# Kernel optimization log

Measured on AMD Instinct MI355X. Metric: run time of the kernel, lower is better.

## Reference

```python
import jax, jax.numpy as jnp
import numpy as np

ACT_BITS = 8  # global_act_bit in the original repo
QMAX = float(2 ** ACT_BITS - 1)


def _fake_quant_asym(x):
    """Asymmetric per-tensor fake quantization (weight_quant_fn, activate=True)."""
    mx = jnp.max(x)
    mn = jnp.min(x)
    scale = (mx - mn) / QMAX
    zp = jnp.round(-mn / scale)
    q = jnp.clip(jnp.round(x / scale) + zp, 0.0, QMAX)
    return (q - zp) * scale


def setup_inputs() -> dict:
    key = jax.random.key(0)
    kx, kq, kr, kl, ks = jax.random.split(key, 5)
    B, S, IN, OUT, R = 32, 1024, 1152, 1152, 64
    x = jax.random.normal(kx, (B, S, IN), dtype=jnp.float32)
    quant_w = jax.random.normal(kq, (OUT, IN), dtype=jnp.float32) * 0.02  # quant.weight
    right_w = jax.random.normal(kr, (R, IN), dtype=jnp.float32) * 0.02   # right.weight
    left_w = jax.random.normal(kl, (OUT, R), dtype=jnp.float32) * 0.02   # left.weight
    bias = jnp.zeros((OUT,), dtype=jnp.float32)
    scales = jax.random.uniform(ks, (IN,), dtype=jnp.float32, minval=0.5, maxval=2.0)
    return {"x": x, "quant_w": quant_w, "right_w": right_w,
            "left_w": left_w, "bias": bias, "scales": scales}


def reference(x, quant_w, right_w, left_w, bias, scales):
    # inference path, merge=False: smooth-quant style scale division, then
    # asymmetric per-tensor fake quant, then quant GEMM + low-rank SVD adapter.
    xs = x / scales                                   # [B,S,IN] elementwise
    xq = _fake_quant_asym(xs)                         # global max/min fake quant
    hx = jnp.einsum('bsi,oi->bso', xq, quant_w)       # quantized linear
    lrx = jnp.einsum('bsr,or->bso',
                     jnp.einsum('bsi,ri->bsr', xq, right_w), left_w)  # low-rank
    return hx + lrx + bias
```

## Files before the change

### kernel.cpp

```cpp
#include <hip/hip_runtime.h>
#include <hip/hip_bf16.h>
#include <stdint.h>

#define M_DIM   32768
#define IN_DIM  1152
#define OUT_DIM 1152
#define R_DIM   64
#define QMAXF   255.0f

#define MM_BLOCKS 2048
#define WP_BLOCKS (OUT_DIM * IN_DIM / 256)
#define QBLOCKS   4096

typedef float  f32x4  __attribute__((ext_vector_type(4)));
typedef __bf16 bf16x8 __attribute__((ext_vector_type(8)));

static __device__ __forceinline__ unsigned short f2bf(float f) {
    unsigned int u = __float_as_uint(f);
    unsigned int r = (u + 0x7fffu + ((u >> 16) & 1u)) >> 16;
    return (unsigned short)r;
}

__global__ __launch_bounds__(256) void k_prep(const float* __restrict__ x,
                                              const float* __restrict__ scales,
                                              const float* __restrict__ qw,
                                              const float* __restrict__ rw,
                                              const float* __restrict__ lw,
                                              unsigned short* __restrict__ wc,
                                              float* __restrict__ rs,
                                              float* __restrict__ partials) {
    __shared__ __align__(16) float srs[IN_DIM];
    __shared__ float smn[4], smx[4];

    if (blockIdx.x < MM_BLOCKS) {
        for (int c = threadIdx.x; c < IN_DIM; c += 256)
            srs[c] = 1.0f / scales[c];
        __syncthreads();

        const int n4 = (M_DIM * IN_DIM) / 4;
        int tid = blockIdx.x * 256 + threadIdx.x;
        const int stride = MM_BLOCKS * 256;
        float mn = 3.4e38f, mx = -3.4e38f;
        for (int i4 = tid; i4 < n4; i4 += stride) {
            int i = i4 * 4;
            float4 xv = *(const float4*)(x + i);
            int c = i % IN_DIM;
            float4 sv = *(const float4*)(&srs[c]);
            float a0 = xv.x * sv.x, a1 = xv.y * sv.y;
            float a2 = xv.z * sv.z, a3 = xv.w * sv.w;
            mn = fminf(mn, fminf(fminf(a0, a1), fminf(a2, a3)));
            mx = fmaxf(mx, fmaxf(fmaxf(a0, a1), fmaxf(a2, a3)));
        }
        #pragma unroll
        for (int off = 32; off > 0; off >>= 1) {
            mn = fminf(mn, __shfl_down(mn, off));
            mx = fmaxf(mx, __shfl_down(mx, off));
        }
        int lane = threadIdx.x & 63, wv = threadIdx.x >> 6;
        if (lane == 0) { smn[wv] = mn; smx[wv] = mx; }
        __syncthreads();
        if (threadIdx.x == 0) {
            float bmn = fminf(fminf(smn[0], smn[1]), fminf(smn[2], smn[3]));
            float bmx = fmaxf(fmaxf(smx[0], smx[1]), fmaxf(smx[2], smx[3]));
            partials[blockIdx.x * 2]     = bmn;
            partials[blockIdx.x * 2 + 1] = bmx;
        }
    } else {
        int idx = (blockIdx.x - MM_BLOCKS) * 256 + threadIdx.x;
        if (idx < IN_DIM) rs[idx] = 1.0f / scales[idx];
        int o = idx / IN_DIM;
        int i = idx - o * IN_DIM;
        float acc = qw[idx];
        #pragma unroll 8
        for (int r = 0; r < R_DIM; r++)
            acc += lw[o * R_DIM + r] * rw[r * IN_DIM + i];
        wc[idx] = f2bf(acc);
    }
}

__global__ __launch_bounds__(256) void k_quantf(const float* __restrict__ x,
                                                const float* __restrict__ rs,
                                                const float* __restrict__ partials,
                                                float* __restrict__ qp,
                                                unsigned short* __restrict__ xq) {
    __shared__ float smn[4], smx[4];
    __shared__ float s_lo, s_hi, s_rqs;

    float mn = 3.4e38f, mx = -3.4e38f;
    for (int i = threadIdx.x; i < MM_BLOCKS; i += 256) {
        mn = fminf(mn, partials[i * 2]);
        mx = fmaxf(mx, partials[i * 2 + 1]);
    }
    #pragma unroll
    for (int off = 32; off > 0; off >>= 1) {
        mn = fminf(mn, __shfl_down(mn, off));
        mx = fmaxf(mx, __shfl_down(mx, off));
    }
    int lane = threadIdx.x & 63, wv = threadIdx.x >> 6;
    if (lane == 0) { smn[wv] = mn; smx[wv] = mx; }
    __syncthreads();
    if (threadIdx.x == 0) {
        float bmn = fminf(fminf(smn[0], smn[1]), fminf(smn[2], smn[3]));
        float bmx = fmaxf(fmaxf(smx[0], smx[1]), fmaxf(smx[2], smx[3]));
        float qs = (bmx - bmn) / QMAXF;
        float zp = rintf(-bmn / qs);
        s_lo  = -zp;
        s_hi  = QMAXF - zp;
        s_rqs = 1.0f / qs;
        if (blockIdx.x == 0) qp[0] = qs;
    }
    __syncthreads();
    const float lo = s_lo, hi = s_hi, rqs = s_rqs;

    const int n4 = (M_DIM * IN_DIM) / 4;
    int tid = blockIdx.x * 256 + threadIdx.x;
    const int stride = QBLOCKS * 256;
    for (int i4 = tid; i4 < n4; i4 += stride) {
        int i = i4 * 4;
        float4 xv = *(const float4*)(x + i);
        int c = i % IN_DIM;
        float4 sv = *(const float4*)(rs + c);
        float a[4] = { (xv.x * sv.x) * rqs, (xv.y * sv.y) * rqs,
                       (xv.z * sv.z) * rqs, (xv.w * sv.w) * rqs };
        ushort4 o;
        unsigned short* op = (unsigned short*)&o;
        #pragma unroll
        for (int j = 0; j < 4; j++) {
            float q = rintf(a[j]);
            q = fminf(fmaxf(q, lo), hi);
            op[j] = f2bf(q);
        }
        *(ushort4*)(xq + i) = o;
    }
}

#define BM 128
#define BN 128
#define BK 32

__global__ __launch_bounds__(256) void k_gemm(const unsigned short* __restrict__ A,
                                              const unsigned short* __restrict__ Bw,
                                              const float* __restrict__ bias,
                                              const float* __restrict__ qp,
                                              float* __restrict__ C) {
    __shared__ __align__(16) unsigned short As[BM * BK];
    __shared__ __align__(16) unsigned short Bs[BN * BK];
    const int tid = threadIdx.x;
    const int bm = blockIdx.x, bn = blockIdx.y;
    const int K = IN_DIM, N = OUT_DIM;

    const int r0 = tid >> 2;
    const int c0 = (tid & 3) * 8;
    const unsigned short* ga0 = A  + (size_t)(bm * BM + r0) * K + c0;
    const unsigned short* ga1 = ga0 + (size_t)64 * K;
    const unsigned short* gb0 = Bw + (size_t)(bn * BN + r0) * K + c0;
    const unsigned short* gb1 = gb0 + (size_t)64 * K;
    unsigned short* lA0 = As + tid * 8;
    unsigned short* lA1 = As + tid * 8 + 2048;
    unsigned short* lB0 = Bs + tid * 8;
    unsigned short* lB1 = Bs + tid * 8 + 2048;

    f32x4 acc[4][4];
    #pragma unroll
    for (int mi = 0; mi < 4; mi++)
        #pragma unroll
        for (int ni = 0; ni < 4; ni++)
            acc[mi][ni] = (f32x4)0.0f;

    const int lane = tid & 63, wv = tid >> 6;
    const int wm = (wv & 1) * 64;
    const int wn = (wv >> 1) * 64;
    const int l16 = lane & 15, l4 = lane >> 4;
    const bf16x8* Asv = (const bf16x8*)As;
    const bf16x8* Bsv = (const bf16x8*)Bs;
    const int afo = (wm + l16) * 4 + l4;
    const int bfo = (wn + l16) * 4 + l4;

    for (int k0 = 0; k0 < K; k0 += BK) {
        __builtin_amdgcn_global_load_lds(
            (const __attribute__((address_space(1))) unsigned int*)(ga0 + k0),
            (__attribute__((address_space(3))) unsigned int*)lA0, 16, 0, 0);
        __builtin_amdgcn_global_load_lds(
            (const __attribute__((address_space(1))) unsigned int*)(ga1 + k0),
            (__attribute__((address_space(3))) unsigned int*)lA1, 16, 0, 0);
        __builtin_amdgcn_global_load_lds(
            (const __attribute__((address_space(1))) unsigned int*)(gb0 + k0),
            (__attribute__((address_space(3))) unsigned int*)lB0, 16, 0, 0);
        __builtin_amdgcn_global_load_lds(
            (const __attribute__((address_space(1))) unsigned int*)(gb1 + k0),
            (__attribute__((address_space(3))) unsigned int*)lB1, 16, 0, 0);
        __syncthreads();

        bf16x8 af[4], bf[4];
        #pragma unroll
        for (int mi = 0; mi < 4; mi++) af[mi] = Asv[afo + mi * 64];
        #pragma unroll
        for (int ni = 0; ni < 4; ni++) bf[ni] = Bsv[bfo + ni * 64];
        #pragma unroll
        for (int mi = 0; mi < 4; mi++)
            #pragma unroll
            for (int ni = 0; ni < 4; ni++)
                acc[mi][ni] = __builtin_amdgcn_mfma_f32_16x16x32_bf16(
                    af[mi], bf[ni], acc[mi][ni], 0, 0, 0);
        __syncthreads();
    }

    const float qs = qp[0];
    #pragma unroll
    for (int mi = 0; mi < 4; mi++) {
        int row0 = bm * BM + wm + mi * 16 + l4 * 4;
        #pragma unroll
        for (int ni = 0; ni < 4; ni++) {
            int col = bn * BN + wn + ni * 16 + l16;
            float bv = bias[col];
            #pragma unroll
            for (int r = 0; r < 4; r++)
                C[(size_t)(row0 + r) * N + col] = acc[mi][ni][r] * qs + bv;
        }
    }
}

extern "C" void kernel_launch(void* const* d_in, const int* in_sizes, int n_in,
                              void* d_out, int out_size, void* d_ws, size_t ws_size,
                              hipStream_t stream) {
    const float* x      = (const float*)d_in[0];
    const float* qw     = (const float*)d_in[1];
    const float* rw     = (const float*)d_in[2];
    const float* lw     = (const float*)d_in[3];
    const float* bias   = (const float*)d_in[4];
    const float* scales = (const float*)d_in[5];

    char* ws = (char*)d_ws;
    unsigned short* xq = (unsigned short*)ws;
    unsigned short* wc = (unsigned short*)(ws + 75497472);
    float* partials    = (float*)(ws + 75497472 + 2654208);
    float* qp          = (float*)(ws + 75497472 + 2654208 + 16384);
    float* rs          = (float*)(ws + 75497472 + 2654208 + 16384 + 64);

    k_prep  <<<MM_BLOCKS + WP_BLOCKS, 256, 0, stream>>>(x, scales, qw, rw, lw,
                                                        wc, rs, partials);
    k_quantf<<<QBLOCKS, 256, 0, stream>>>(x, rs, partials, qp, xq);

    dim3 grid(M_DIM / BM, OUT_DIM / BN);
    k_gemm<<<grid, 256, 0, stream>>>(xq, wc, bias, qp, (float*)d_out);
}
```

Baseline: 418.1 us.

## Swizzle LDS tiles, overlap next-tile loads with MFMA, vectorize epilogue stores

The GEMM now XOR-swizzles the LDS column chunk per row pair to reduce bank conflicts on fragment reads. It issues the global-to-LDS loads for the next K tile right after the fragments are pulled into registers, so the loads overlap with that tile's MFMAs, still using a single buffer. The MFMA operands are swapped so each lane holds four consecutive columns, which lets the epilogue write float4 stores and read bias as a vector. The cost is an extra barrier per iteration, and the single LDS buffer leaves only the MFMA work to hide load latency.

```diff
diff --git a/kernel.cpp b/kernel.cpp
--- a/kernel.cpp
+++ b/kernel.cpp
@@ -137,6 +137,7 @@
 #define BM 128
 #define BN 128
 #define BK 32
+#define NT (IN_DIM / BK)
 
 __global__ __launch_bounds__(256) void k_gemm(const unsigned short* __restrict__ A,
                                               const unsigned short* __restrict__ Bw,
@@ -150,7 +151,7 @@
     const int K = IN_DIM, N = OUT_DIM;
 
     const int r0 = tid >> 2;
-    const int c0 = (tid & 3) * 8;
+    const int c0 = (((tid & 3) ^ ((r0 >> 1) & 3))) * 8;
     const unsigned short* ga0 = A  + (size_t)(bm * BM + r0) * K + c0;
     const unsigned short* ga1 = ga0 + (size_t)64 * K;
     const unsigned short* gb0 = Bw + (size_t)(bn * BN + r0) * K + c0;
@@ -173,22 +174,24 @@
     const int l16 = lane & 15, l4 = lane >> 4;
     const bf16x8* Asv = (const bf16x8*)As;
     const bf16x8* Bsv = (const bf16x8*)Bs;
-    const int afo = (wm + l16) * 4 + l4;
-    const int bfo = (wn + l16) * 4 + l4;
-
-    for (int k0 = 0; k0 < K; k0 += BK) {
-        __builtin_amdgcn_global_load_lds(
-            (const __attribute__((address_space(1))) unsigned int*)(ga0 + k0),
-            (__attribute__((address_space(3))) unsigned int*)lA0, 16, 0, 0);
-        __builtin_amdgcn_global_load_lds(
-            (const __attribute__((address_space(1))) unsigned int*)(ga1 + k0),
-            (__attribute__((address_space(3))) unsigned int*)lA1, 16, 0, 0);
-        __builtin_amdgcn_global_load_lds(
-            (const __attribute__((address_space(1))) unsigned int*)(gb0 + k0),
-            (__attribute__((address_space(3))) unsigned int*)lB0, 16, 0, 0);
-        __builtin_amdgcn_global_load_lds(
-            (const __attribute__((address_space(1))) unsigned int*)(gb1 + k0),
-            (__attribute__((address_space(3))) unsigned int*)lB1, 16, 0, 0);
+    const int swz = ((l16 >> 1) & 3);
+    const int afo = (wm + l16) * 4 + (l4 ^ swz);
+    const int bfo = (wn + l16) * 4 + (l4 ^ swz);
+
+    __builtin_amdgcn_global_load_lds(
+        (const __attribute__((address_space(1))) unsigned int*)ga0,
+        (__attribute__((address_space(3))) unsigned int*)lA0, 16, 0, 0);
+    __builtin_amdgcn_global_load_lds(
+        (const __attribute__((address_space(1))) unsigned int*)ga1,
+        (__attribute__((address_space(3))) unsigned int*)lA1, 16, 0, 0);
+    __builtin_amdgcn_global_load_lds(
+        (const __attribute__((address_space(1))) unsigned int*)gb0,
+        (__attribute__((address_space(3))) unsigned int*)lB0, 16, 0, 0);
+    __builtin_amdgcn_global_load_lds(
+        (const __attribute__((address_space(1))) unsigned int*)gb1,
+        (__attribute__((address_space(3))) unsigned int*)lB1, 16, 0, 0);
+
+    for (int t = 0; t < NT; ++t) {
         __syncthreads();
 
         bf16x8 af[4], bf[4];
@@ -196,26 +199,49 @@
         for (int mi = 0; mi < 4; mi++) af[mi] = Asv[afo + mi * 64];
         #pragma unroll
         for (int ni = 0; ni < 4; ni++) bf[ni] = Bsv[bfo + ni * 64];
+
+        __syncthreads();
+
+        if (t + 1 < NT) {
+            const int kc = (t + 1) * BK;
+            __builtin_amdgcn_global_load_lds(
+                (const __attribute__((address_space(1))) unsigned int*)(ga0 + kc),
+                (__attribute__((address_space(3))) unsigned int*)lA0, 16, 0, 0);
+            __builtin_amdgcn_global_load_lds(
+                (const __attribute__((address_space(1))) unsigned int*)(ga1 + kc),
+                (__attribute__((address_space(3))) unsigned int*)lA1, 16, 0, 0);
+            __builtin_amdgcn_global_load_lds(
+                (const __attribute__((address_space(1))) unsigned int*)(gb0 + kc),
+                (__attribute__((address_space(3))) unsigned int*)lB0, 16, 0, 0);
+            __builtin_amdgcn_global_load_lds(
+                (const __attribute__((address_space(1))) unsigned int*)(gb1 + kc),
+                (__attribute__((address_space(3))) unsigned int*)lB1, 16, 0, 0);
+        }
+
         #pragma unroll
         for (int mi = 0; mi < 4; mi++)
             #pragma unroll
             for (int ni = 0; ni < 4; ni++)
                 acc[mi][ni] = __builtin_amdgcn_mfma_f32_16x16x32_bf16(
-                    af[mi], bf[ni], acc[mi][ni], 0, 0, 0);
-        __syncthreads();
+                    bf[ni], af[mi], acc[mi][ni], 0, 0, 0);
     }
 
     const float qs = qp[0];
     #pragma unroll
     for (int mi = 0; mi < 4; mi++) {
-        int row0 = bm * BM + wm + mi * 16 + l4 * 4;
+        const int row = bm * BM + wm + mi * 16 + l16;
+        float* crow = C + (size_t)row * N;
         #pragma unroll
         for (int ni = 0; ni < 4; ni++) {
-            int col = bn * BN + wn + ni * 16 + l16;
-            float bv = bias[col];
-            #pragma unroll
-            for (int r = 0; r < 4; r++)
-                C[(size_t)(row0 + r) * N + col] = acc[mi][ni][r] * qs + bv;
+            const int colb = bn * BN + wn + ni * 16 + l4 * 4;
+            f32x4 bv = *(const f32x4*)(bias + colb);
+            f32x4 v  = acc[mi][ni];
+            f32x4 out;
+            out[0] = v[0] * qs + bv[0];
+            out[1] = v[1] * qs + bv[1];
+            out[2] = v[2] * qs + bv[2];
+            out[3] = v[3] * qs + bv[3];
+            *(f32x4*)(crow + colb) = out;
         }
     }
 }
```

Result: slower. 426.6 us (+2.0%).
